# Kernel optimization log

Measured on AMD Instinct MI355X. Metric: run time of the kernel, lower is better.

## Reference

```python
import jax, jax.numpy as jnp
import numpy as np

B, N, E, D, H, C, U = 512, 256, 1024, 256, 256, 8, 64
MARGIN_T, RISK_T, SCALE = 0.2, 0.6, 0.1
NEG = -1.0e9


def setup_inputs() -> dict:
    key = jax.random.key(0)
    ks = jax.random.split(key, 30)
    s = 0.02
    inp = dict(
        features=jax.random.normal(ks[0], (B, D), jnp.float32),
        centered_scores=jax.random.normal(ks[1], (B, N), jnp.float32),
        margin=jax.random.uniform(ks[2], (B,), jnp.float32),
        boundary_risk=jax.random.uniform(ks[3], (B,), jnp.float32),
        edge_sensitivity=jax.random.normal(ks[4], (B, E), jnp.float32),
        coords=jax.random.normal(ks[5], (B, N, C), jnp.float32),
        uncertainty=jax.random.uniform(ks[6], (B, U), jnp.float32),
        Wc1=jax.random.normal(ks[7], (D, H), jnp.float32) * s,
        bc1=jnp.zeros((H,), jnp.float32),
        Wc2=jax.random.normal(ks[8], (H, H), jnp.float32) * s,
        bc2=jnp.zeros((H,), jnp.float32),
        Wn1=jax.random.normal(ks[9], (H + C + 2, H), jnp.float32) * s,
        bn1=jnp.zeros((H,), jnp.float32),
        Wn2=jax.random.normal(ks[10], (H, 1), jnp.float32) * s,
        bn2=jnp.zeros((1,), jnp.float32),
        We1=jax.random.normal(ks[11], (H + C + 2, H), jnp.float32) * s,
        be1=jnp.zeros((H,), jnp.float32),
        We2=jax.random.normal(ks[12], (H, 1), jnp.float32) * s,
        be2=jnp.zeros((1,), jnp.float32),
        Wg=jax.random.normal(ks[13], (H, 1), jnp.float32) * s,
        bg=jnp.zeros((1,), jnp.float32),
        action_mask=jax.random.bernoulli(ks[14], 0.8, (B, N)),
        edge_mask=jax.random.bernoulli(ks[15], 0.8, (B, E)),
        actions=jax.random.randint(ks[16], (B, N), 0, U, jnp.int32),
        edges=jax.random.randint(ks[17], (B, E, 2), 0, N, jnp.int32),
    )
    return inp


def _mlp2(x, W1, b1, W2, b2):
    return jax.nn.relu(x @ W1 + b1) @ W2 + b2


def reference(features, centered_scores, margin, boundary_risk, edge_sensitivity,
              coords, uncertainty, Wc1, bc1, Wc2, bc2, Wn1, bn1, Wn2, bn2,
              We1, be1, We2, be2, Wg, bg, action_mask, edge_mask, actions, edges):
    amf = action_mask.astype(jnp.float32)
    emf = edge_mask.astype(jnp.float32)

    # context MLP
    h = jax.nn.relu(jax.nn.relu(features @ Wc1 + bc1) @ Wc2 + bc2)  # [B,H]

    low_margin = (margin < MARGIN_T).astype(jnp.float32)
    high_risk = (boundary_risk > RISK_T).astype(jnp.float32)
    learned_gate = jax.nn.sigmoid((h @ Wg + bg)[:, 0])
    refine_gate = jnp.maximum(jnp.maximum(low_margin, high_risk),
                              (learned_gate > 0.5).astype(jnp.float32))  # [B]

    # node features: [B,N,H+C+2]
    act = jnp.clip(actions, 0, U - 1)
    unc_g = jnp.take_along_axis(uncertainty, act, axis=1)  # [B,N]
    h_n = jnp.broadcast_to(h[:, None, :], (B, N, H))
    node_feats = jnp.concatenate(
        [h_n, coords, centered_scores[..., None], unc_g[..., None]], axis=-1)
    node_delta = _mlp2(node_feats, Wn1, bn1, Wn2, bn2)[..., 0] * amf  # [B,N]

    # edge features: gather src/dst coords
    e = jnp.clip(edges, 0, N - 1)
    src_c = jnp.take_along_axis(coords, e[:, :, 0:1], axis=1)  # [B,E,C]
    dst_c = jnp.take_along_axis(coords, e[:, :, 1:2], axis=1)  # [B,E,C]
    h_e = jnp.broadcast_to(h[:, None, :], (B, E, H))
    edge_feats = jnp.concatenate(
        [h_e, dst_c - src_c, edge_sensitivity[..., None], emf[..., None]], axis=-1)
    edge_delta = _mlp2(edge_feats, We1, be1, We2, be2)[..., 0] * emf  # [B,E]

    gate_node = refine_gate[:, None]
    refined_scores = (centered_scores + gate_node * SCALE * node_delta) * amf
    denom = jnp.clip(amf.sum(-1, keepdims=True), 1.0, None)  # [B,1]
    refined_scores = (refined_scores - refined_scores.sum(-1, keepdims=True) / denom) * amf

    refined_edge = (edge_sensitivity + gate_node * SCALE * edge_delta) * emf

    masked_top = jnp.where(action_mask, refined_scores, NEG)
    top_vals, top_idx = jax.lax.top_k(masked_top, 2)
    refined_margin = top_vals[:, 0] - top_vals[:, 1]

    # masked per-batch variance of refined_edge (biased), 0 if <=1 valid entry
    cnt = emf.sum(-1)
    cnt_c = jnp.clip(cnt, 1.0, None)
    mean = (refined_edge * emf).sum(-1) / cnt_c
    var = (emf * (refined_edge - mean[:, None]) ** 2).sum(-1) / cnt_c
    edge_var = jnp.where(cnt > 1.0, var, 0.0)

    unc_term = (unc_g * amf).sum(-1) / denom[:, 0]
    refined_risk = jnp.clip(
        jax.nn.sigmoid(-refined_margin) + 0.2 * edge_var + 0.1 * unc_term, 0.0, 1.0)

    return (refined_scores, refined_margin, refined_edge,
            top_idx[:, 0], refined_risk, refine_gate)
```

## Files before the change

kernel.cpp:

```cpp
#include <hip/hip_runtime.h>
#include <math.h>

#define B 512
#define N 256
#define E 1024
#define D 256
#define H 256
#define C 8
#define U 64

typedef __fp16 h2 __attribute__((ext_vector_type(2)));
union UF { float f; h2 h; unsigned u; };

__device__ __forceinline__ float bc_f(h2 h) { UF u; u.h = h; return u.f; }
__device__ __forceinline__ h2 bc_h(float f) { UF u; u.f = f; return u.h; }

#if __has_builtin(__builtin_amdgcn_cvt_pkrtz)
__device__ __forceinline__ h2 pkh(float a, float b) { return __builtin_amdgcn_cvt_pkrtz(a, b); }
#else
__device__ __forceinline__ h2 pkh(float a, float b) { h2 r; r.x = (__fp16)a; r.y = (__fp16)b; return r; }
#endif

#if __has_builtin(__builtin_amdgcn_fdot2)
__device__ __forceinline__ float FDOT2(h2 a, h2 b, float c) { return __builtin_amdgcn_fdot2(a, b, c, false); }
#else
__device__ __forceinline__ float FDOT2(h2 a, h2 b, float c) {
    return fmaf((float)a.x, (float)b.x, fmaf((float)a.y, (float)b.y, c));
}
#endif

__device__ __forceinline__ float mask_val(const void* m, long i, int flag) {
    if (flag == 1) return ((const unsigned char*)m)[i] ? 1.f : 0.f;
    if (flag == 2) return (((const float*)m)[i] != 0.f) ? 1.f : 0.f;
    return ((const int*)m)[i] ? 1.f : 0.f;
}

__device__ __forceinline__ float block_sum(float v, float* red) {
    int t = threadIdx.x;
    red[t] = v; __syncthreads();
    for (int s = 128; s > 0; s >>= 1) {
        if (t < s) red[t] += red[t + s];
        __syncthreads();
    }
    float r = red[0]; __syncthreads();
    return r;
}

__global__ __launch_bounds__(512) void k_h(
    const float* __restrict__ feat,
    const float* __restrict__ Wc1, const float* __restrict__ bc1,
    const float* __restrict__ Wc2, const float* __restrict__ bc2,
    const float* __restrict__ Wn1, const float* __restrict__ bn1,
    const float* __restrict__ We1, const float* __restrict__ be1,
    const float* __restrict__ Wg,  const float* __restrict__ bg,
    const float* __restrict__ margin, const float* __restrict__ brisk,
    const unsigned int* __restrict__ amask_words,
    float* __restrict__ base_n, float* __restrict__ base_e,
    float* __restrict__ out_gate, int* __restrict__ flag,
    float* __restrict__ node_delta, float* __restrict__ out2)
{
    __shared__ __align__(16) float sF[2][256];
    __shared__ __align__(16) float sH[2][256];
    __shared__ float red[512];
    __shared__ int cls0, cls1;

    int t = threadIdx.x;
    int w = t >> 8;
    int c = t & 255;
    int b0 = blockIdx.x * 2;
    int b = b0 + w;

    {
        int idx = blockIdx.x * 512 + t;
        node_delta[idx] = 0.f;
        ((float4*)out2)[idx] = make_float4(0.f, 0.f, 0.f, 0.f);
    }

    if (blockIdx.x == 0) {
        if (t == 0) { cls0 = 0; cls1 = 0; }
        __syncthreads();
        if (t < 256) {
            unsigned int wd = amask_words[t];
            if (wd != 0u && wd != 1u) {
                if (wd == 0x3f800000u) atomicOr(&cls1, 1);
                else                   atomicOr(&cls0, 1);
            }
        }
        __syncthreads();
        if (t == 0) *flag = cls0 ? 1 : (cls1 ? 2 : 0);
    }

    sF[w][c] = feat[(long)b * D + c];
    __syncthreads();

    {
        float acc[4] = {bc1[c], 0.f, 0.f, 0.f};
        const float* Wp = Wc1 + c;
        for (int d0 = 0; d0 < D; d0 += 16) {
            float wv[16];
            #pragma unroll
            for (int k = 0; k < 16; k++) wv[k] = Wp[(long)(d0 + k) * H];
            #pragma unroll
            for (int k = 0; k < 16; k++)
                acc[k & 3] = fmaf(sF[w][d0 + k], wv[k], acc[k & 3]);
        }
        sH[w][c] = fmaxf((acc[0] + acc[1]) + (acc[2] + acc[3]), 0.f);
    }
    __syncthreads();

    {
        float acc[4] = {bc2[c], 0.f, 0.f, 0.f};
        const float* Wp = Wc2 + c;
        for (int d0 = 0; d0 < H; d0 += 16) {
            float wv[16];
            #pragma unroll
            for (int k = 0; k < 16; k++) wv[k] = Wp[(long)(d0 + k) * H];
            #pragma unroll
            for (int k = 0; k < 16; k++)
                acc[k & 3] = fmaf(sH[w][d0 + k], wv[k], acc[k & 3]);
        }
        float a = fmaxf((acc[0] + acc[1]) + (acc[2] + acc[3]), 0.f);
        __syncthreads();
        sF[w][c] = a;
    }
    __syncthreads();

    red[t] = sF[w][c] * Wg[c];
    __syncthreads();
    for (int s = 128; s > 0; s >>= 1) {
        if (c < s) red[t] += red[t + s];
        __syncthreads();
    }
    if (c == 0) {
        float lg = 1.f / (1.f + expf(-(red[t] + bg[0])));
        out_gate[b] = ((margin[b] < 0.2f) || (brisk[b] > 0.6f) || (lg > 0.5f)) ? 1.f : 0.f;
    }

    {
        const float* W3  = w ? (We1 + c) : (Wn1 + c);
        float bias       = w ? be1[c]    : bn1[c];
        float* dst       = w ? base_e    : base_n;
        float aA[2] = {bias, 0.f};
        float aB[2] = {bias, 0.f};
        for (int d0 = 0; d0 < H; d0 += 16) {
            float wv[16];
            #pragma unroll
            for (int k = 0; k < 16; k++) wv[k] = W3[(long)(d0 + k) * H];
            #pragma unroll
            for (int k = 0; k < 16; k++) {
                aA[k & 1] = fmaf(sF[0][d0 + k], wv[k], aA[k & 1]);
                aB[k & 1] = fmaf(sF[1][d0 + k], wv[k], aB[k & 1]);
            }
        }
        dst[(long)b0 * H + c]       = aA[0] + aA[1];
        dst[(long)(b0 + 1) * H + c] = aB[0] + aB[1];
    }
}

__global__ __launch_bounds__(256, 2) void k_ne(
    const float* __restrict__ cs, const float* __restrict__ coords,
    const float* __restrict__ unc, const int* __restrict__ actions,
    const float* __restrict__ Wn1, const float* __restrict__ Wn2,
    const float* __restrict__ base_n,
    const float* __restrict__ es, const int* __restrict__ edges,
    const float* __restrict__ We1, const float* __restrict__ We2,
    const float* __restrict__ base_e,
    const float* __restrict__ gate,
    float* __restrict__ node_delta, float* __restrict__ out2)
{
    __shared__ __align__(16) float smem[3840];
    int t = threadIdx.x;
    int w = t >> 6, lane = t & 63;

    if (blockIdx.x < 512) {
        int rg = blockIdx.x >> 2;
        int jq = blockIdx.x & 3;
        int b0 = rg * 4;
        float* pack = smem;
        float* sB   = smem + 768;

        {
            int i = t;
            #pragma unroll
            for (int s = 0; s < 3; s++, i += 256) {
                int j = i / 12, k = i - j * 12;
                int jj = jq * 64 + j;
                float v;
                if (k < 10)       v = Wn1[(long)(H + k) * H + jj];
                else if (k == 10) v = Wn2[jj];
                else              v = 0.f;
                pack[i] = v;
            }
            int r = t >> 6, j = t & 63;
            sB[r * 64 + j] = base_n[(long)(b0 + r) * H + jq * 64 + j];
        }
        __syncthreads();

        int b = b0 + w;
        float g = gate[b];
        if (g != 0.f) {
            float f8v[4], ug[4], acc[4];
            float f0[4], f1[4], f2[4], f3[4], f4[4], f5[4], f6[4], f7[4];
            #pragma unroll
            for (int q = 0; q < 4; q++) {
                int n = q * 64 + lane;
                const float4* cp = (const float4*)(coords + ((long)b * N + n) * C);
                float4 c0 = cp[0], c1 = cp[1];
                f0[q] = c0.x; f1[q] = c0.y; f2[q] = c0.z; f3[q] = c0.w;
                f4[q] = c1.x; f5[q] = c1.y; f6[q] = c1.z; f7[q] = c1.w;
                f8v[q] = cs[(long)b * N + n];
                int a = actions[(long)b * N + n];
                a = min(max(a, 0), U - 1);
                ug[q] = unc[(long)b * U + a];
                acc[q] = 0.f;
            }

            const float* sBw = sB + w * 64;
            #pragma unroll 4
            for (int j = 0; j < 64; j++) {
                const float* pj = pack + j * 12;
                float4 wa = *(const float4*)(pj);
                float4 wb = *(const float4*)(pj + 4);
                float4 wc = *(const float4*)(pj + 8);
                float bse = sBw[j];
                #pragma unroll
                for (int q = 0; q < 4; q++) {
                    float zA = fmaf(f0[q], wa.x, bse);
                    zA = fmaf(f1[q], wa.y, zA);
                    zA = fmaf(f2[q], wa.z, zA);
                    zA = fmaf(f3[q], wa.w, zA);
                    float zB = f4[q] * wb.x;
                    zB = fmaf(f5[q], wb.y, zB);
                    zB = fmaf(f6[q], wb.z, zB);
                    zB = fmaf(f7[q], wb.w, zB);
                    zB = fmaf(f8v[q], wc.x, zB);
                    zB = fmaf(ug[q], wc.y, zB);
                    acc[q] = fmaf(fmaxf(zA + zB, 0.f), wc.z, acc[q]);
                }
            }

            #pragma unroll
            for (int q = 0; q < 4; q++)
                atomicAdd(&node_delta[(long)b * N + q * 64 + lane], acc[q]);
        }
    } else {
        int eb = blockIdx.x - 512;
        int b = eb >> 2, jq = eb & 3;
        float g = gate[b];
        if (g == 0.f) return;

        float*  A4 = smem;
        float2* B2 = (float2*)(smem + 256);
        float*  sC = smem + 768;

        {
            const float4* g4 = (const float4*)(coords + (long)b * N * C);
            float4 c0 = g4[2 * t], c1 = g4[2 * t + 1];
            float4* d0 = (float4*)(sC + t * 12);
            d0[0] = c0; d0[1] = c1;
        }
        if (t < 64) {
            int j = jq * 64 + t;
            float w0 = We1[(long)(H + 0) * H + j];
            float w1 = We1[(long)(H + 1) * H + j];
            float w2 = We1[(long)(H + 2) * H + j];
            float w3 = We1[(long)(H + 3) * H + j];
            float w4 = We1[(long)(H + 4) * H + j];
            float w5 = We1[(long)(H + 5) * H + j];
            float w6 = We1[(long)(H + 6) * H + j];
            float w7 = We1[(long)(H + 7) * H + j];
            float w8 = We1[(long)(H + 8) * H + j];
            float w9 = We1[(long)(H + 9) * H + j];
            float we2 = We2[j];
            float bse = base_e[(long)b * H + j] + w9;
            float4 av;
            av.x = bc_f(pkh(w0, w1)); av.y = bc_f(pkh(w2, w3));
            av.z = bc_f(pkh(w4, w5)); av.w = bc_f(pkh(w6, w7));
            ((float4*)A4)[t] = av;
            B2[t] = make_float2(bc_f(pkh(w8, we2)), bse);
        }
        __syncthreads();

        float p01[4], p23[4], p45[4], p67[4], pes[4], acc[4];
        #pragma unroll
        for (int q = 0; q < 4; q++) {
            long idx = (long)b * E + w * 256 + q * 64 + lane;
            int2 ev = ((const int2*)edges)[idx];
            int s0 = min(max(ev.x, 0), N - 1);
            int d0 = min(max(ev.y, 0), N - 1);
            const float4* cs4 = (const float4*)(sC + s0 * 12);
            const float4* cd4 = (const float4*)(sC + d0 * 12);
            float4 sa = cs4[0], sb = cs4[1];
            float4 da = cd4[0], db = cd4[1];
            p01[q] = bc_f(pkh(da.x - sa.x, da.y - sa.y));
            p23[q] = bc_f(pkh(da.z - sa.z, da.w - sa.w));
            p45[q] = bc_f(pkh(db.x - sb.x, db.y - sb.y));
            p67[q] = bc_f(pkh(db.z - sb.z, db.w - sb.w));
            pes[q] = bc_f(pkh(es[idx], 0.f));
            acc[q] = 0.f;
        }

        const float4* A4v = (const float4*)A4;
        #pragma unroll 4
        for (int j = 0; j < 64; j++) {
            float4 av = A4v[j];
            float2 bv = B2[j];
            h2 w01 = bc_h(av.x), w23 = bc_h(av.y);
            h2 w45 = bc_h(av.z), w67 = bc_h(av.w);
            h2 w8x = bc_h(bv.x);
            float we2f = (float)(w8x.y);
            float bse = bv.y;
            #pragma unroll
            for (int q = 0; q < 4; q++) {
                float z = FDOT2(bc_h(p01[q]), w01, bse);
                z = FDOT2(bc_h(p23[q]), w23, z);
                z = FDOT2(bc_h(p45[q]), w45, z);
                z = FDOT2(bc_h(p67[q]), w67, z);
                z = FDOT2(bc_h(pes[q]), w8x, z);
                acc[q] = fmaf(fmaxf(z, 0.f), we2f, acc[q]);
            }
        }

        #pragma unroll
        for (int q = 0; q < 4; q++)
            atomicAdd(&out2[(long)b * E + w * 256 + q * 64 + lane], acc[q]);
    }
}

__global__ __launch_bounds__(256) void k_finrisk(
    const void* __restrict__ amask, const void* __restrict__ emask,
    const int* __restrict__ actions, const float* __restrict__ unc,
    const float* __restrict__ cs, const float* __restrict__ es,
    const float* __restrict__ bn2, const float* __restrict__ be2,
    const float* __restrict__ gate, const int* __restrict__ flagp,
    const float* __restrict__ node_delta,
    float* __restrict__ out0, float* __restrict__ out1,
    float* __restrict__ out2, float* __restrict__ out3,
    float* __restrict__ out4)
{
    __shared__ float red[256];
    __shared__ int ridx[256];
    __shared__ float sRiskbase;
    int t = threadIdx.x;
    int b = blockIdx.x;
    int flag = *flagp;
    float g = gate[b];

    {
        float am = mask_val(amask, (long)b * N + t, flag);
        float csv = cs[(long)b * N + t];
        int a = actions[(long)b * N + t];
        a = min(max(a, 0), U - 1);
        float ug = unc[(long)b * U + a];
        float nd = (node_delta[(long)b * N + t] + bn2[0]) * am;
        float raw = (csv + g * 0.1f * nd) * am;

        float sum = block_sum(raw, red);
        float cnt = block_sum(am, red);
        float denom = fmaxf(cnt, 1.f);
        float rs = (raw - sum / denom) * am;
        out0[(long)b * N + t] = rs;

        float masked = (am != 0.f) ? rs : -1e9f;

        red[t] = masked; ridx[t] = t; __syncthreads();
        for (int s = 128; s > 0; s >>= 1) {
            if (t < s) {
                float o = red[t + s]; int oi = ridx[t + s];
                if (o > red[t] || (o == red[t] && oi < ridx[t])) { red[t] = o; ridx[t] = oi; }
            }
            __syncthreads();
        }
        float v1 = red[0]; int i1 = ridx[0]; __syncthreads();

        red[t] = (t == i1) ? -1e9f : masked; __syncthreads();
        for (int s = 128; s > 0; s >>= 1) {
            if (t < s) red[t] = fmaxf(red[t], red[t + s]);
            __syncthreads();
        }
        float v2 = red[0]; __syncthreads();
        float rmargin = v1 - v2;

        float su = block_sum(ug * am, red);

        if (t == 0) {
            out1[b] = rmargin;
            out3[b] = (float)i1;
            float sig = 1.f / (1.f + expf(rmargin));
            sRiskbase = sig + 0.1f * (su / denom);
        }
    }
    __syncthreads();

    {
        float be2v = be2[0];
        float re[4], emv[4];
        #pragma unroll
        for (int q = 0; q < 4; q++) {
            long idx = (long)b * E + t + 256 * q;
            emv[q] = mask_val(emask, idx, flag);
            float delta = out2[idx] + be2v;
            float r = es[idx] + g * 0.1f * delta;
            re[q] = (emv[q] != 0.f) ? r : 0.f;
            out2[idx] = re[q];
        }

        float S1 = 0.f, ce = 0.f;
        #pragma unroll
        for (int q = 0; q < 4; q++) { S1 += re[q]; ce += emv[q]; }
        float S1t = block_sum(S1, red);
        float cet = block_sum(ce, red);
        float mean = S1t / fmaxf(cet, 1.f);
        float v = 0.f;
        #pragma unroll
        for (int q = 0; q < 4; q++) {
            float dd = re[q] - mean;
            v = fmaf(emv[q] * dd, dd, v);
        }
        float vt = block_sum(v, red);
        if (t == 0) {
            float var = vt / fmaxf(cet, 1.f);
            float ev = (cet > 1.f) ? var : 0.f;
            float r = sRiskbase + 0.2f * ev;
            out4[b] = fminf(fmaxf(r, 0.f), 1.f);
        }
    }
}

extern "C" void kernel_launch(void* const* d_in, const int* in_sizes, int n_in,
                              void* d_out, int out_size, void* d_ws, size_t ws_size,
                              hipStream_t stream) {
    const float* feat   = (const float*)d_in[0];
    const float* cs     = (const float*)d_in[1];
    const float* marg   = (const float*)d_in[2];
    const float* brisk  = (const float*)d_in[3];
    const float* es     = (const float*)d_in[4];
    const float* coords = (const float*)d_in[5];
    const float* unc    = (const float*)d_in[6];
    const float* Wc1    = (const float*)d_in[7];
    const float* bc1    = (const float*)d_in[8];
    const float* Wc2    = (const float*)d_in[9];
    const float* bc2    = (const float*)d_in[10];
    const float* Wn1    = (const float*)d_in[11];
    const float* bn1    = (const float*)d_in[12];
    const float* Wn2    = (const float*)d_in[13];
    const float* bn2    = (const float*)d_in[14];
    const float* We1    = (const float*)d_in[15];
    const float* be1    = (const float*)d_in[16];
    const float* We2    = (const float*)d_in[17];
    const float* be2    = (const float*)d_in[18];
    const float* Wg     = (const float*)d_in[19];
    const float* bg     = (const float*)d_in[20];
    const void*  amask  = d_in[21];
    const void*  emask  = d_in[22];
    const int*   actions= (const int*)d_in[23];
    const int*   edges  = (const int*)d_in[24];

    float* out0 = (float*)d_out;
    float* out1 = out0 + (long)B * N;
    float* out2 = out1 + B;
    float* out3 = out2 + (long)B * E;
    float* out4 = out3 + B;
    float* out5 = out4 + B;

    float* base_n     = (float*)d_ws;
    float* base_e     = base_n + (long)B * H;
    float* node_delta = base_e + (long)B * H;
    int*   flag       = (int*)(node_delta + (long)B * N);

    k_h<<<B / 2, 512, 0, stream>>>(feat, Wc1, bc1, Wc2, bc2, Wn1, bn1, We1, be1,
                                   Wg, bg, marg, brisk,
                                   (const unsigned int*)amask,
                                   base_n, base_e, out5, flag,
                                   node_delta, out2);
    k_ne<<<512 + 4 * B, 256, 0, stream>>>(cs, coords, unc, actions,
                                          Wn1, Wn2, base_n,
                                          es, edges,
                                          We1, We2, base_e,
                                          out5, node_delta, out2);
    k_finrisk<<<B, 256, 0, stream>>>(amask, emask, actions, unc, cs, es,
                                     bn2, be2, out5, flag, node_delta,
                                     out0, out1, out2, out3, out4);
}
```

Measured before the change: 74.34 us.

## Replace block tree reductions in final kernel with wave shuffles and wave specialization

The final risk kernel now runs 512 threads per batch row. One wavefront handles the node scores, the mean, the top-2 selection and the uncertainty term, while four other wavefronts handle the edge refinement and variance. They run concurrently and reduce with cross-lane shuffles instead of many shared-memory tree reductions, each guarded by a barrier. This removes most __syncthreads calls and serial dependency chains in the tail kernel. Separately, the edge MLP inner loop gains a redundant dot-product chain whose result is overwritten; the compiler should eliminate it, but it is stray code.

Measured after the change: 69.95 us. -5.9%, faster.

```diff
diff --git a/kernel.cpp b/kernel.cpp
--- a/kernel.cpp
+++ b/kernel.cpp
@@ -33,17 +33,6 @@
     if (flag == 1) return ((const unsigned char*)m)[i] ? 1.f : 0.f;
     if (flag == 2) return (((const float*)m)[i] != 0.f) ? 1.f : 0.f;
     return ((const int*)m)[i] ? 1.f : 0.f;
-}
-
-__device__ __forceinline__ float block_sum(float v, float* red) {
-    int t = threadIdx.x;
-    red[t] = v; __syncthreads();
-    for (int s = 128; s > 0; s >>= 1) {
-        if (t < s) red[t] += red[t + s];
-        __syncthreads();
-    }
-    float r = red[0]; __syncthreads();
-    return r;
 }
 
 __global__ __launch_bounds__(512) void k_h(
@@ -315,7 +304,10 @@
                 float z = FDOT2(bc_h(p01[q]), w01, bse);
                 z = FDOT2(bc_h(p23[q]), w23, z);
                 z = FDOT2(bc_h(p45[q]), w45, z);
-                z = FDOT2(bc_h(p67[q]), w67, z);
+                z = FDOT2(bc_h(p67[q]), w8x, z);
+                acc[q] = acc[q];
+                z = FDOT2(bc_h(p67[q]), w67, FDOT2(bc_h(p45[q]), w45,
+                    FDOT2(bc_h(p23[q]), w23, FDOT2(bc_h(p01[q]), w01, bse))));
                 z = FDOT2(bc_h(pes[q]), w8x, z);
                 acc[q] = fmaf(fmaxf(z, 0.f), we2f, acc[q]);
             }
@@ -327,7 +319,7 @@
     }
 }
 
-__global__ __launch_bounds__(256) void k_finrisk(
+__global__ __launch_bounds__(512) void k_fin2(
     const void* __restrict__ amask, const void* __restrict__ emask,
     const int* __restrict__ actions, const float* __restrict__ unc,
     const float* __restrict__ cs, const float* __restrict__ es,
@@ -338,92 +330,130 @@
     float* __restrict__ out2, float* __restrict__ out3,
     float* __restrict__ out4)
 {
-    __shared__ float red[256];
-    __shared__ int ridx[256];
-    __shared__ float sRiskbase;
+    __shared__ float sRisk;
+    __shared__ float sS1[8], sCe[8], sVar[8];
     int t = threadIdx.x;
+    int w = t >> 6, lane = t & 63;
     int b = blockIdx.x;
     int flag = *flagp;
     float g = gate[b];
 
-    {
-        float am = mask_val(amask, (long)b * N + t, flag);
-        float csv = cs[(long)b * N + t];
-        int a = actions[(long)b * N + t];
-        a = min(max(a, 0), U - 1);
-        float ug = unc[(long)b * U + a];
-        float nd = (node_delta[(long)b * N + t] + bn2[0]) * am;
-        float raw = (csv + g * 0.1f * nd) * am;
-
-        float sum = block_sum(raw, red);
-        float cnt = block_sum(am, red);
-        float denom = fmaxf(cnt, 1.f);
-        float rs = (raw - sum / denom) * am;
-        out0[(long)b * N + t] = rs;
-
-        float masked = (am != 0.f) ? rs : -1e9f;
-
-        red[t] = masked; ridx[t] = t; __syncthreads();
-        for (int s = 128; s > 0; s >>= 1) {
-            if (t < s) {
-                float o = red[t + s]; int oi = ridx[t + s];
-                if (o > red[t] || (o == red[t] && oi < ridx[t])) { red[t] = o; ridx[t] = oi; }
-            }
-            __syncthreads();
-        }
-        float v1 = red[0]; int i1 = ridx[0]; __syncthreads();
-
-        red[t] = (t == i1) ? -1e9f : masked; __syncthreads();
-        for (int s = 128; s > 0; s >>= 1) {
-            if (t < s) red[t] = fmaxf(red[t], red[t + s]);
-            __syncthreads();
-        }
-        float v2 = red[0]; __syncthreads();
-        float rmargin = v1 - v2;
-
-        float su = block_sum(ug * am, red);
-
-        if (t == 0) {
+    float re[4], emv[4];
+
+    if (w == 0) {
+        float b2v = bn2[0];
+        float raw[4], amv[4], ug[4];
+        #pragma unroll
+        for (int q = 0; q < 4; q++) {
+            long idx = (long)b * N + q * 64 + lane;
+            amv[q] = mask_val(amask, idx, flag);
+            float csv = cs[idx];
+            int a = actions[idx];
+            a = min(max(a, 0), U - 1);
+            ug[q] = unc[(long)b * U + a];
+            float nd = (node_delta[idx] + b2v) * amv[q];
+            raw[q] = (csv + g * 0.1f * nd) * amv[q];
+        }
+
+        float s = 0.f, cn = 0.f, su = 0.f;
+        #pragma unroll
+        for (int q = 0; q < 4; q++) {
+            s += raw[q]; cn += amv[q]; su += ug[q] * amv[q];
+        }
+        #pragma unroll
+        for (int m = 1; m < 64; m <<= 1) {
+            s  += __shfl_xor(s, m);
+            cn += __shfl_xor(cn, m);
+            su += __shfl_xor(su, m);
+        }
+        float denom = fmaxf(cn, 1.f);
+        float mu = s / denom;
+
+        float masked[4];
+        #pragma unroll
+        for (int q = 0; q < 4; q++) {
+            float rs = (raw[q] - mu) * amv[q];
+            out0[(long)b * N + q * 64 + lane] = rs;
+            masked[q] = (amv[q] != 0.f) ? rs : -1e9f;
+        }
+
+        float v1 = masked[0]; int i1 = lane; float v2 = -1e9f;
+        #pragma unroll
+        for (int q = 1; q < 4; q++) {
+            float mv = masked[q]; int mi = q * 64 + lane;
+            if (mv > v1) { v2 = v1; v1 = mv; i1 = mi; }
+            else v2 = fmaxf(v2, mv);
+        }
+        #pragma unroll
+        for (int m = 1; m < 64; m <<= 1) {
+            float ov1 = __shfl_xor(v1, m);
+            int   oi1 = __shfl_xor(i1, m);
+            float ov2 = __shfl_xor(v2, m);
+            bool ow = (ov1 > v1) || (ov1 == v1 && oi1 < i1);
+            float lv  = ow ? v1 : ov1;
+            float wv2 = ow ? ov2 : v2;
+            if (ow) { v1 = ov1; i1 = oi1; }
+            v2 = fmaxf(lv, wv2);
+        }
+
+        if (lane == 0) {
+            float rmargin = v1 - v2;
             out1[b] = rmargin;
             out3[b] = (float)i1;
             float sig = 1.f / (1.f + expf(rmargin));
-            sRiskbase = sig + 0.1f * (su / denom);
-        }
-    }
-    __syncthreads();
-
-    {
+            sRisk = sig + 0.1f * (su / denom);
+            sS1[0] = 0.f; sCe[0] = 0.f;
+        }
+    } else if (w >= 4) {
         float be2v = be2[0];
-        float re[4], emv[4];
+        int eq = w - 4;
+        float S1 = 0.f, ce = 0.f;
         #pragma unroll
         for (int q = 0; q < 4; q++) {
-            long idx = (long)b * E + t + 256 * q;
+            long idx = (long)b * E + eq * 256 + q * 64 + lane;
             emv[q] = mask_val(emask, idx, flag);
             float delta = out2[idx] + be2v;
             float r = es[idx] + g * 0.1f * delta;
             re[q] = (emv[q] != 0.f) ? r : 0.f;
             out2[idx] = re[q];
-        }
-
-        float S1 = 0.f, ce = 0.f;
-        #pragma unroll
-        for (int q = 0; q < 4; q++) { S1 += re[q]; ce += emv[q]; }
-        float S1t = block_sum(S1, red);
-        float cet = block_sum(ce, red);
-        float mean = S1t / fmaxf(cet, 1.f);
+            S1 += re[q]; ce += emv[q];
+        }
+        #pragma unroll
+        for (int m = 1; m < 64; m <<= 1) {
+            S1 += __shfl_xor(S1, m);
+            ce += __shfl_xor(ce, m);
+        }
+        if (lane == 0) { sS1[w] = S1; sCe[w] = ce; }
+    } else {
+        if (lane == 0) { sS1[w] = 0.f; sCe[w] = 0.f; }
+    }
+    __syncthreads();
+
+    float S1t = sS1[4] + sS1[5] + sS1[6] + sS1[7];
+    float cet = sCe[4] + sCe[5] + sCe[6] + sCe[7];
+    float mean = S1t / fmaxf(cet, 1.f);
+
+    if (w >= 4) {
         float v = 0.f;
         #pragma unroll
         for (int q = 0; q < 4; q++) {
             float dd = re[q] - mean;
             v = fmaf(emv[q] * dd, dd, v);
         }
-        float vt = block_sum(v, red);
-        if (t == 0) {
-            float var = vt / fmaxf(cet, 1.f);
-            float ev = (cet > 1.f) ? var : 0.f;
-            float r = sRiskbase + 0.2f * ev;
-            out4[b] = fminf(fmaxf(r, 0.f), 1.f);
-        }
+        #pragma unroll
+        for (int m = 1; m < 64; m <<= 1) v += __shfl_xor(v, m);
+        if (lane == 0) sVar[w] = v;
+    } else {
+        if (lane == 0) sVar[w] = 0.f;
+    }
+    __syncthreads();
+
+    if (t == 0) {
+        float vt = sVar[4] + sVar[5] + sVar[6] + sVar[7];
+        float var = vt / fmaxf(cet, 1.f);
+        float ev = (cet > 1.f) ? var : 0.f;
+        float r = sRisk + 0.2f * ev;
+        out4[b] = fminf(fmaxf(r, 0.f), 1.f);
     }
 }
 
@@ -478,7 +508,7 @@
                                           es, edges,
                                           We1, We2, base_e,
                                           out5, node_delta, out2);
-    k_finrisk<<<B, 256, 0, stream>>>(amask, emask, actions, unc, cs, es,
-                                     bn2, be2, out5, flag, node_delta,
-                                     out0, out1, out2, out3, out4);
+    k_fin2<<<B, 512, 0, stream>>>(amask, emask, actions, unc, cs, es,
+                                  bn2, be2, out5, flag, node_delta,
+                                  out0, out1, out2, out3, out4);
 }
```
